# Kernel optimization log

Hardware: AMD Instinct MI355X
Metric: run time of the kernel (lower is better)

## Reference

```python
import jax, jax.numpy as jnp
import numpy as np


def setup_inputs() -> dict:
    key = jax.random.key(0)
    k1, k2 = jax.random.split(key)
    B, F = 131072, 32
    LOCAL_DIM, RANK, UNITS = 2, 10, 8
    X = jax.random.normal(k1, (B, F), dtype=jnp.float32)
    kernel = jax.random.normal(k2, (LOCAL_DIM, RANK, F, UNITS), dtype=jnp.float32) * 0.24  # ~glorot for fan sizes here
    return {"X": X, "kernel": kernel}


def reference(X, kernel):
    # X: [B, F]; kernel: [local_dim, rank, F, units]
    local_dim = kernel.shape[0]
    # powers X^0 .. X^(local_dim-1), stacked on last axis -> [B, F, local_dim]
    powers = jnp.stack([X ** p for p in range(local_dim)], axis=-1)
    # L2-normalize over the power axis (matches tf.sqrt(reduce_sum(x**2)))
    norms = jnp.sqrt(jnp.sum(powers * powers, axis=-1, keepdims=True))
    x = powers / norms  # [B, F, local_dim]
    # per-feature matmul across all units at once: [B, F, rank, units]
    t = jnp.einsum('bfd,drfu->bfru', x, kernel)
    # hadamard product over features, then sum over CP rank -> [B, units]
    out = jnp.sum(jnp.prod(t, axis=1), axis=1)
    return out  # activation is linear (None)
```

## Files before the change

### kernel.cpp

```cpp
#include <hip/hip_runtime.h>


typedef float f32x2 __attribute__((ext_vector_type(2)));
typedef float f32x4 __attribute__((ext_vector_type(4)));

#define F 32
#define RANK 10
#define UNITS 8
#define RPW 32
#define WPB 4

__global__ __launch_bounds__(64 * WPB) void cp_based_kernel(
    const float* __restrict__ X,
    const float* __restrict__ K,
    float* __restrict__ out,
    int B)
{
    const int lane = threadIdx.x;
    const int u = lane & 7;
    const int s = lane >> 3;
    const int wy = __builtin_amdgcn_readfirstlane(threadIdx.y);
    const int wid = blockIdx.x * WPB + wy;
    const long row0 = (long)wid * RPW;

    f32x4 xb[4];
    {
        const float* xp = X + (row0 + (lane >> 1)) * F + 16 * (lane & 1);
#pragma unroll
        for (int j = 0; j < 4; ++j)
            xb[j] = *reinterpret_cast<const f32x4*>(xp + 4 * j);
    }

    f32x2 k0a[16], k1a[16], k0b[16], k1b[16];
    {
        const int r1 = s;
#pragma unroll
        for (int fp = 0; fp < 16; ++fp) {
            const int f0 = 2 * fp;
            k0a[fp] = f32x2{K[((0 * RANK + r1) * F + f0) * UNITS + u],
                            K[((0 * RANK + r1) * F + f0 + 1) * UNITS + u]};
            k1a[fp] = f32x2{K[((1 * RANK + r1) * F + f0) * UNITS + u],
                            K[((1 * RANK + r1) * F + f0 + 1) * UNITS + u]};
        }
    }
    if (s < 2) {
        const int r2 = 8 + s;
#pragma unroll
        for (int fp = 0; fp < 16; ++fp) {
            const int f0 = 2 * fp;
            k0b[fp] = f32x2{K[((0 * RANK + r2) * F + f0) * UNITS + u],
                            K[((0 * RANK + r2) * F + f0 + 1) * UNITS + u]};
            k1b[fp] = f32x2{K[((1 * RANK + r2) * F + f0) * UNITS + u],
                            K[((1 * RANK + r2) * F + f0 + 1) * UNITS + u]};
        }
    } else {
#pragma unroll
        for (int fp = 0; fp < 16; ++fp) {
            k0b[fp] = f32x2{0.f, 0.f};
            k1b[fp] = f32x2{0.f, 0.f};
        }
    }
#pragma unroll
    for (int fp = 0; fp < 16; ++fp) {
        asm volatile("" : "+v"(k0a[fp]), "+v"(k1a[fp]));
        asm volatile("" : "+v"(k0b[fp]), "+v"(k1b[fp]));
    }

    float rsqv;
    {
        f32x4 na = xb[0] * xb[0] + f32x4{1.f, 1.f, 1.f, 1.f};
        f32x4 nb = xb[1] * xb[1] + f32x4{1.f, 1.f, 1.f, 1.f};
        f32x4 nc = xb[2] * xb[2] + f32x4{1.f, 1.f, 1.f, 1.f};
        f32x4 nd = xb[3] * xb[3] + f32x4{1.f, 1.f, 1.f, 1.f};
        f32x4 nv = (na * nb) * (nc * nd);
        float npl = (nv[0] * nv[1]) * (nv[2] * nv[3]);
        npl *= __shfl_xor(npl, 1);
        rsqv = __builtin_amdgcn_rsqf(npl);
    }

    const f32x2 one2 = {1.f, 1.f};

    auto COMPUTE = [&](const f32x4* xq, int i) {
        f32x2 ta[4], tb[4];
#pragma unroll
        for (int q = 0; q < 4; ++q) {
            f32x2 xp = {xq[q >> 1][2 * (q & 1)], xq[q >> 1][2 * (q & 1) + 1]};
            ta[q] = xp * k1a[q] + k0a[q];
            tb[q] = xp * k1b[q] + k0b[q];
        }
#pragma unroll
        for (int fp = 4; fp < 16; ++fp) {
            const int q = fp & 3;
            f32x2 xp = {xq[fp >> 1][2 * (fp & 1)], xq[fp >> 1][2 * (fp & 1) + 1]};
            ta[q] *= xp * k1a[fp] + k0a[fp];
            tb[q] *= xp * k1b[fp] + k0b[fp];
        }
        ta[0] *= ta[1]; ta[2] *= ta[3]; ta[0] *= ta[2];
        tb[0] *= tb[1]; tb[2] *= tb[3]; tb[0] *= tb[2];
        float P = __builtin_fmaf(tb[0][0], tb[0][1], ta[0][0] * ta[0][1]);
        P += __shfl_xor(P, 8);
        P += __shfl_xor(P, 16);
        P += __shfl_xor(P, 32);
        float srsq = __uint_as_float(
            __builtin_amdgcn_readlane(__float_as_uint(rsqv), 2 * i));
        if (s == 0)
            out[(row0 + i) * UNITS + u] = P * srsq;
    };

    auto LOADROW = [&](f32x4* dst, int i) {
        const f32x4* xr4 = reinterpret_cast<const f32x4*>(X + (row0 + i) * F);
#pragma unroll
        for (int j = 0; j < 8; ++j) dst[j] = xr4[j];
    };

    f32x4 xA[8], xB[8];
    LOADROW(xA, 0);
#pragma unroll
    for (int i = 0; i < RPW; i += 2) {
        LOADROW(xB, i + 1);
        COMPUTE(xA, i);
        LOADROW(xA, i + 2 < RPW ? i + 2 : RPW - 1);
        COMPUTE(xB, i + 1);
    }
}

extern "C" void kernel_launch(void* const* d_in, const int* in_sizes, int n_in,
                              void* d_out, int out_size, void* d_ws, size_t ws_size,
                              hipStream_t stream) {
    const float* X = (const float*)d_in[0];
    const float* K = (const float*)d_in[1];
    float* out = (float*)d_out;
    const int B = in_sizes[0] / F;

    dim3 block(64, WPB);
    dim3 grid(B / (RPW * WPB));
    hipLaunchKernelGGL(cp_based_kernel, grid, block, 0, stream, X, K, out, B);
}
```

Measured before the change: 32.39 us.

## Broadcast X rows via readlane from coalesced registers instead of per-row global reloads

Each row's 32 features are now taken from the coalesced per-wave register load using v_readlane scalar broadcasts, so rows are no longer re-read from global memory with double-buffered per-lane loads. The row loop is no longer fully unrolled, launch bounds request two blocks per CU, and the asm barriers on the kernel registers are no longer volatile. This removes the redundant global and cache traffic for X and frees the xA/xB register buffers, at the cost of 32 readlanes per row serialized through scalar registers and less unrolling.

```diff
diff --git a/kernel.cpp b/kernel.cpp
--- a/kernel.cpp
+++ b/kernel.cpp
@@ -10,7 +10,7 @@
 #define RPW 32
 #define WPB 4
 
-__global__ __launch_bounds__(64 * WPB) void cp_based_kernel(
+__global__ __launch_bounds__(64 * WPB, 2) void cp_based_kernel(
     const float* __restrict__ X,
     const float* __restrict__ K,
     float* __restrict__ out,
@@ -62,65 +62,65 @@
     }
 #pragma unroll
     for (int fp = 0; fp < 16; ++fp) {
-        asm volatile("" : "+v"(k0a[fp]), "+v"(k1a[fp]));
-        asm volatile("" : "+v"(k0b[fp]), "+v"(k1b[fp]));
+        asm("" : "+v"(k0a[fp]), "+v"(k1a[fp]));
+        asm("" : "+v"(k0b[fp]), "+v"(k1b[fp]));
     }
 
     float rsqv;
     {
-        f32x4 na = xb[0] * xb[0] + f32x4{1.f, 1.f, 1.f, 1.f};
-        f32x4 nb = xb[1] * xb[1] + f32x4{1.f, 1.f, 1.f, 1.f};
-        f32x4 nc = xb[2] * xb[2] + f32x4{1.f, 1.f, 1.f, 1.f};
-        f32x4 nd = xb[3] * xb[3] + f32x4{1.f, 1.f, 1.f, 1.f};
+        const f32x4 one4 = {1.f, 1.f, 1.f, 1.f};
+        f32x4 na = xb[0] * xb[0] + one4;
+        f32x4 nb = xb[1] * xb[1] + one4;
+        f32x4 nc = xb[2] * xb[2] + one4;
+        f32x4 nd = xb[3] * xb[3] + one4;
         f32x4 nv = (na * nb) * (nc * nd);
         float npl = (nv[0] * nv[1]) * (nv[2] * nv[3]);
         npl *= __shfl_xor(npl, 1);
         rsqv = __builtin_amdgcn_rsqf(npl);
     }
 
-    const f32x2 one2 = {1.f, 1.f};
+    for (int i = 0; i < RPW; ++i) {
+        const int lbase = 2 * i;
 
-    auto COMPUTE = [&](const f32x4* xq, int i) {
+        float sx[32];
+#pragma unroll
+        for (int fp = 0; fp < 16; ++fp) {
+            const int half = fp >> 3;
+            const int fl = (2 * fp) & 15;
+            const int j = fl >> 2, c = fl & 3;
+            sx[2 * fp] = __uint_as_float(__builtin_amdgcn_readlane(
+                __float_as_uint(xb[j][c]), lbase + half));
+            sx[2 * fp + 1] = __uint_as_float(__builtin_amdgcn_readlane(
+                __float_as_uint(xb[j][c + 1]), lbase + half));
+        }
+
         f32x2 ta[4], tb[4];
 #pragma unroll
         for (int q = 0; q < 4; ++q) {
-            f32x2 xp = {xq[q >> 1][2 * (q & 1)], xq[q >> 1][2 * (q & 1) + 1]};
+            f32x2 xp = {sx[2 * q], sx[2 * q + 1]};
             ta[q] = xp * k1a[q] + k0a[q];
             tb[q] = xp * k1b[q] + k0b[q];
         }
 #pragma unroll
         for (int fp = 4; fp < 16; ++fp) {
             const int q = fp & 3;
-            f32x2 xp = {xq[fp >> 1][2 * (fp & 1)], xq[fp >> 1][2 * (fp & 1) + 1]};
+            f32x2 xp = {sx[2 * fp], sx[2 * fp + 1]};
             ta[q] *= xp * k1a[fp] + k0a[fp];
             tb[q] *= xp * k1b[fp] + k0b[fp];
         }
         ta[0] *= ta[1]; ta[2] *= ta[3]; ta[0] *= ta[2];
         tb[0] *= tb[1]; tb[2] *= tb[3]; tb[0] *= tb[2];
+
         float P = __builtin_fmaf(tb[0][0], tb[0][1], ta[0][0] * ta[0][1]);
+
         P += __shfl_xor(P, 8);
         P += __shfl_xor(P, 16);
         P += __shfl_xor(P, 32);
-        float srsq = __uint_as_float(
-            __builtin_amdgcn_readlane(__float_as_uint(rsqv), 2 * i));
+
+        const float srsq = __uint_as_float(
+            __builtin_amdgcn_readlane(__float_as_uint(rsqv), lbase));
         if (s == 0)
             out[(row0 + i) * UNITS + u] = P * srsq;
-    };
-
-    auto LOADROW = [&](f32x4* dst, int i) {
-        const f32x4* xr4 = reinterpret_cast<const f32x4*>(X + (row0 + i) * F);
-#pragma unroll
-        for (int j = 0; j < 8; ++j) dst[j] = xr4[j];
-    };
-
-    f32x4 xA[8], xB[8];
-    LOADROW(xA, 0);
-#pragma unroll
-    for (int i = 0; i < RPW; i += 2) {
-        LOADROW(xB, i + 1);
-        COMPUTE(xA, i);
-        LOADROW(xA, i + 2 < RPW ? i + 2 : RPW - 1);
-        COMPUTE(xB, i + 1);
     }
 }
 
```

Measured after the change: 44.87 us. 1.39x slower.
